# Optimization experiments

Hardware: AMD Instinct MI355X
Metric: run time of the kernel (lower is better)

Reference implementation:

```python
import jax, jax.numpy as jnp
import numpy as np

N = 524288          # batch of embedded samples
K = 16              # num_mixtures
D = 16              # dimension_embedding


def setup_inputs() -> dict:
    key = jax.random.key(0)
    k_s, k_phi, k_mu, k_sig = jax.random.split(key, 4)
    samples = jax.random.normal(k_s, (N, D), dtype=jnp.float32)
    # Mixture.__init__: Phi ~ U[0,1) scalar per mixture, mu ~ 2*U[0,1)-0.5
    Phi = jax.random.uniform(k_phi, (K,), dtype=jnp.float32)
    mu = 2.0 * jax.random.uniform(k_mu, (K, D), dtype=jnp.float32) - 0.5
    # Sigma init is identity in the original; use a well-conditioned SPD
    # perturbation of identity so inverse/det are non-trivial but stable.
    A = jax.random.normal(k_sig, (K, D, D), dtype=jnp.float32)
    Sigma = jnp.eye(D, dtype=jnp.float32)[None] + 0.1 * jnp.einsum('kij,klj->kil', A, A) / D
    return {"samples": samples, "Phi": Phi, "mu": mu, "Sigma": Sigma}


def reference(samples, Phi, mu, Sigma):
    # Faithful batched version of GMM.forward: sum_k Phi_k * exp(-0.5 * diff^T Sigma_k^{-1} diff) / sqrt(2*pi*det(Sigma_k)), then -log.
    inv_sigma = jnp.linalg.inv(Sigma)                      # [K, D, D]
    det_sigma = jnp.linalg.det(Sigma)                      # [K]
    diff = samples[None, :, :] - mu[:, None, :]            # [K, N, D]
    quad = jnp.einsum('knd,kde,kne->kn', diff, inv_sigma, diff)  # [K, N]
    # NOTE: original normalizes by sqrt(2*pi*det), not (2*pi)^{D/2}*sqrt(det);
    # we reproduce the original math exactly.
    norm = jnp.sqrt(2.0 * jnp.pi * det_sigma)[:, None]     # [K, 1]
    pdf = Phi[:, None] * jnp.exp(-0.5 * quad) / norm       # [K, N]
    return -jnp.log(jnp.sum(pdf, axis=0))                  # [N]
```

## Files before the change

### kernel.cpp

```cpp
#include <hip/hip_runtime.h>
#include <hip/hip_bf16.h>
#include <math.h>

#define KMIX 16
#define DIM  16
#define TPW  8

typedef _Float16 half8 __attribute__((ext_vector_type(8)));
typedef float    f32x4 __attribute__((ext_vector_type(4)));

__global__ __launch_bounds__(64) void gmm_precompute(
    const float* __restrict__ Phi, const float* __restrict__ mu,
    const float* __restrict__ Sigma,
    _Float16* __restrict__ wsA, float* __restrict__ wsC)
{
    const int lane = threadIdx.x;
    const int r    = lane & 15;
    const int base = lane & 48;
    const int k    = blockIdx.x * 4 + (lane >> 4);

    float l[DIM];
    {
        const float4* p = (const float4*)(Sigma + k * 256 + r * 16);
        const float4 a = p[0], b = p[1], c = p[2], d = p[3];
        l[0]=a.x;  l[1]=a.y;  l[2]=a.z;  l[3]=a.w;
        l[4]=b.x;  l[5]=b.y;  l[6]=b.z;  l[7]=b.w;
        l[8]=c.x;  l[9]=c.y;  l[10]=c.z; l[11]=c.w;
        l[12]=d.x; l[13]=d.y; l[14]=d.z; l[15]=d.w;
    }

    float rd_own = 0.0f;
    #pragma unroll
    for (int j = 0; j < DIM; ++j) {
        const float dj  = __builtin_amdgcn_sqrtf(l[j]);
        const float rdj = __builtin_amdgcn_rcpf(dj);
        if (r == j) { l[j] = dj; rd_own = rdj; }
        const float rdb = __shfl(rdj, base + j, 64);
        if (r > j) l[j] *= rdb;
        #pragma unroll
        for (int c = j + 1; c < DIM; ++c) {
            const float Lcj = __shfl(l[j], base + c, 64);
            if (r >= c) l[c] = fmaf(-l[j], Lcj, l[c]);
        }
    }

    float v[DIM], acc[DIM];
    #pragma unroll
    for (int c = 0; c < DIM; ++c) { v[c] = 0.0f; acc[c] = 0.0f; }
    #pragma unroll
    for (int m = 0; m < DIM; ++m) {
        if (r == m) {
            #pragma unroll
            for (int c = 0; c < DIM; ++c)
                if (c < m) v[c] = -rd_own * acc[c];
            v[m] = rd_own;
        }
        #pragma unroll
        for (int c = 0; c <= m; ++c) {
            const float Vmc = __shfl(v[c], base + m, 64);
            if (r > m) acc[c] = fmaf(l[m], Vmc, acc[c]);
        }
    }

    float prod = rd_own;
    prod *= __shfl_xor(prod, 1, 64);
    prod *= __shfl_xor(prod, 2, 64);
    prod *= __shfl_xor(prod, 4, 64);
    prod *= __shfl_xor(prod, 8, 64);
    if (r == 0) wsC[k] = Phi[k] * 0.3989422804014327f * prod;

    float b = 0.0f;
    {
        const float4* pm = (const float4*)(mu + k * DIM);
        const float4 m0 = pm[0], m1 = pm[1], m2 = pm[2], m3 = pm[3];
        const float mv[DIM] = {m0.x,m0.y,m0.z,m0.w, m1.x,m1.y,m1.z,m1.w,
                               m2.x,m2.y,m2.z,m2.w, m3.x,m3.y,m3.z,m3.w};
        #pragma unroll
        for (int c = 0; c < DIM; ++c) b = fmaf(v[c], mv[c], b);
    }

    half8 h0, h1, h2, h3;
    #pragma unroll
    for (int j = 0; j < 8; ++j) {
        h0[j] = (_Float16)v[j];
        h1[j] = (_Float16)v[8 + j];
        h2[j] = (_Float16)0.0f;
        h3[j] = (_Float16)0.0f;
    }
    h2[0] = (_Float16)(-b);
    half8* W = (half8*)wsA + k * 64;
    W[r]      = h0;
    W[16 + r] = h1;
    W[32 + r] = h2;
    W[48 + r] = h3;
}

__global__ __launch_bounds__(256) void gmm_main(
    const float* __restrict__ samples,
    const _Float16* __restrict__ wsA, const float* __restrict__ wsC,
    float* __restrict__ out, int N, int ntiles)
{
    const int lane = threadIdx.x & 63;
    const int wave = blockIdx.x * (blockDim.x >> 6) + (threadIdx.x >> 6);
    const int n = lane & 15;
    const int quad = lane >> 4;

    half8 afrag[KMIX];
    #pragma unroll
    for (int mix = 0; mix < KMIX; ++mix)
        afrag[mix] = ((const half8*)wsA)[mix * 64 + lane];
    float ck[KMIX];
    #pragma unroll
    for (int mix = 0; mix < KMIX; ++mix) ck[mix] = wsC[mix];

    const f32x4 zero = {0.0f, 0.0f, 0.0f, 0.0f};

    for (int t = 0; t < TPW; ++t) {
        const int tile = wave * TPW + t;
        if (tile >= ntiles) break;
        const int s0 = tile * 16;

        half8 bfrag;
        #pragma unroll
        for (int j = 0; j < 8; ++j) bfrag[j] = (_Float16)0.0f;
        if (quad < 2) {
            int sidx = s0 + n; if (sidx >= N) sidx = N - 1;
            const float4* p = (const float4*)(samples + (size_t)sidx * DIM + quad * 8);
            const float4 u = p[0], v = p[1];
            bfrag[0] = (_Float16)u.x; bfrag[1] = (_Float16)u.y;
            bfrag[2] = (_Float16)u.z; bfrag[3] = (_Float16)u.w;
            bfrag[4] = (_Float16)v.x; bfrag[5] = (_Float16)v.y;
            bfrag[6] = (_Float16)v.z; bfrag[7] = (_Float16)v.w;
        } else if (quad == 2) {
            bfrag[0] = (_Float16)1.0f;
        }

        float sum = 0.0f;
        #pragma unroll
        for (int mix = 0; mix < KMIX; ++mix) {
            const f32x4 d = __builtin_amdgcn_mfma_f32_16x16x32_f16(
                afrag[mix], bfrag, zero, 0, 0, 0);
            float q = d[0] * d[0];
            q = fmaf(d[1], d[1], q);
            q = fmaf(d[2], d[2], q);
            q = fmaf(d[3], d[3], q);
            q += __shfl_xor(q, 16, 64);
            q += __shfl_xor(q, 32, 64);
            sum = fmaf(ck[mix], __expf(-0.5f * q), sum);
        }

        const int sidx = s0 + n;
        if (quad == 0 && sidx < N) out[sidx] = -__logf(sum);
    }
}

extern "C" void kernel_launch(void* const* d_in, const int* in_sizes, int n_in,
                              void* d_out, int out_size, void* d_ws, size_t ws_size,
                              hipStream_t stream)
{
    const float* samples = (const float*)d_in[0];
    const float* Phi     = (const float*)d_in[1];
    const float* mu      = (const float*)d_in[2];
    const float* Sigma   = (const float*)d_in[3];
    float* out = (float*)d_out;
    const int N = in_sizes[0] / DIM;

    _Float16* wsA = (_Float16*)d_ws;
    float* wsC = (float*)((char*)d_ws + KMIX * 64 * 8 * sizeof(_Float16));

    gmm_precompute<<<4, 64, 0, stream>>>(Phi, mu, Sigma, wsA, wsC);

    const int ntiles = (N + 15) / 16;
    const int waves  = (ntiles + TPW - 1) / TPW;
    const int blocks = (waves + 3) / 4;
    gmm_main<<<blocks, 256, 0, stream>>>(samples, wsA, wsC, out, N, ntiles);
}
```

Baseline: 99.86 us.

## Fuse Cholesky precompute into main kernel, redundantly per block via LDS

Removes the separate precompute kernel launch and the global workspace round-trip. Each 256-thread block now runs the Cholesky factorisation and inverse for all 16 mixtures itself, one mixture per 16 lanes, and stores the fp16 MFMA fragments and coefficients in shared memory. The main MFMA loop then reads them from LDS. This saves a launch and the dependency between kernels, but every block repeats the small factorisation work, which adds latency before the main loop and raises register pressure.

```diff
diff --git a/kernel.cpp b/kernel.cpp
--- a/kernel.cpp
+++ b/kernel.cpp
@@ -5,19 +5,25 @@
 #define KMIX 16
 #define DIM  16
 #define TPW  8
-
 typedef _Float16 half8 __attribute__((ext_vector_type(8)));
 typedef float    f32x4 __attribute__((ext_vector_type(4)));
 
-__global__ __launch_bounds__(64) void gmm_precompute(
+__global__ __launch_bounds__(256) void gmm_fused(
+    const float* __restrict__ samples,
     const float* __restrict__ Phi, const float* __restrict__ mu,
     const float* __restrict__ Sigma,
-    _Float16* __restrict__ wsA, float* __restrict__ wsC)
+    float* __restrict__ out, int N, int ntiles)
 {
-    const int lane = threadIdx.x;
+    __shared__ half8 sW[KMIX][64];
+    __shared__ float sCk[KMIX];
+
+    const int tid  = threadIdx.x;
+    const int lane = tid & 63;
     const int r    = lane & 15;
     const int base = lane & 48;
-    const int k    = blockIdx.x * 4 + (lane >> 4);
+    const int wv   = tid >> 6;
+    const int quad = lane >> 4;
+    const int k    = wv * 4 + quad;
 
     float l[DIM];
     {
@@ -67,7 +73,7 @@
     prod *= __shfl_xor(prod, 2, 64);
     prod *= __shfl_xor(prod, 4, 64);
     prod *= __shfl_xor(prod, 8, 64);
-    if (r == 0) wsC[k] = Phi[k] * 0.3989422804014327f * prod;
+    if (r == 0) sCk[k] = Phi[k] * 0.3989422804014327f * prod;
 
     float b = 0.0f;
     {
@@ -79,39 +85,32 @@
         for (int c = 0; c < DIM; ++c) b = fmaf(v[c], mv[c], b);
     }
 
-    half8 h0, h1, h2, h3;
-    #pragma unroll
-    for (int j = 0; j < 8; ++j) {
-        h0[j] = (_Float16)v[j];
-        h1[j] = (_Float16)v[8 + j];
-        h2[j] = (_Float16)0.0f;
-        h3[j] = (_Float16)0.0f;
+    {
+        half8 h0, h1, h2, h3;
+        #pragma unroll
+        for (int j = 0; j < 8; ++j) {
+            h0[j] = (_Float16)v[j];
+            h1[j] = (_Float16)v[8 + j];
+            h2[j] = (_Float16)0.0f;
+            h3[j] = (_Float16)0.0f;
+        }
+        h2[0] = (_Float16)(-b);
+        sW[k][r]      = h0;
+        sW[k][16 + r] = h1;
+        sW[k][32 + r] = h2;
+        sW[k][48 + r] = h3;
     }
-    h2[0] = (_Float16)(-b);
-    half8* W = (half8*)wsA + k * 64;
-    W[r]      = h0;
-    W[16 + r] = h1;
-    W[32 + r] = h2;
-    W[48 + r] = h3;
-}
+    __syncthreads();
 
-__global__ __launch_bounds__(256) void gmm_main(
-    const float* __restrict__ samples,
-    const _Float16* __restrict__ wsA, const float* __restrict__ wsC,
-    float* __restrict__ out, int N, int ntiles)
-{
-    const int lane = threadIdx.x & 63;
-    const int wave = blockIdx.x * (blockDim.x >> 6) + (threadIdx.x >> 6);
     const int n = lane & 15;
-    const int quad = lane >> 4;
+    const int wave = blockIdx.x * 4 + wv;
 
     half8 afrag[KMIX];
     #pragma unroll
-    for (int mix = 0; mix < KMIX; ++mix)
-        afrag[mix] = ((const half8*)wsA)[mix * 64 + lane];
+    for (int mix = 0; mix < KMIX; ++mix) afrag[mix] = sW[mix][lane];
     float ck[KMIX];
     #pragma unroll
-    for (int mix = 0; mix < KMIX; ++mix) ck[mix] = wsC[mix];
+    for (int mix = 0; mix < KMIX; ++mix) ck[mix] = sCk[mix];
 
     const f32x4 zero = {0.0f, 0.0f, 0.0f, 0.0f};
 
@@ -126,11 +125,11 @@
         if (quad < 2) {
             int sidx = s0 + n; if (sidx >= N) sidx = N - 1;
             const float4* p = (const float4*)(samples + (size_t)sidx * DIM + quad * 8);
-            const float4 u = p[0], v = p[1];
+            const float4 u = p[0], w = p[1];
             bfrag[0] = (_Float16)u.x; bfrag[1] = (_Float16)u.y;
             bfrag[2] = (_Float16)u.z; bfrag[3] = (_Float16)u.w;
-            bfrag[4] = (_Float16)v.x; bfrag[5] = (_Float16)v.y;
-            bfrag[6] = (_Float16)v.z; bfrag[7] = (_Float16)v.w;
+            bfrag[4] = (_Float16)w.x; bfrag[5] = (_Float16)w.y;
+            bfrag[6] = (_Float16)w.z; bfrag[7] = (_Float16)w.w;
         } else if (quad == 2) {
             bfrag[0] = (_Float16)1.0f;
         }
@@ -165,13 +164,9 @@
     float* out = (float*)d_out;
     const int N = in_sizes[0] / DIM;
 
-    _Float16* wsA = (_Float16*)d_ws;
-    float* wsC = (float*)((char*)d_ws + KMIX * 64 * 8 * sizeof(_Float16));
-
-    gmm_precompute<<<4, 64, 0, stream>>>(Phi, mu, Sigma, wsA, wsC);
-
     const int ntiles = (N + 15) / 16;
     const int waves  = (ntiles + TPW - 1) / TPW;
     const int blocks = (waves + 3) / 4;
-    gmm_main<<<blocks, 256, 0, stream>>>(samples, wsA, wsC, out, N, ntiles);
+
+    gmm_fused<<<blocks, 256, 0, stream>>>(samples, Phi, mu, Sigma, out, N, ntiles);
 }
```

New measurement: 105.8 us. 1.06x slower.
